# Optimization experiments

Measured on AMD Instinct MI355X. Metric: run time of the kernel, lower is better.

## Reference

```python
import jax, jax.numpy as jnp
import numpy as np

NGRAM = 16
SUB = 512  # bytes per sub-block


def byte2image(block, ngram=NGRAM):
    """block: (B, L) int -> (B, 1, ngram*8, L-ngram) float32 in [-1, 1]."""
    B, L = block.shape
    blk = block.astype(jnp.int32)
    # nxt[:, i] = blk[:, i+1], last column zero
    nxt = jnp.concatenate([blk[:, 1:], jnp.zeros((B, 1), jnp.int32)], axis=1)
    # 8 bit-shifted views of the byte stream
    shifts = jnp.stack(
        [((blk << s) & 255) + ((nxt >> (8 - s)) & 255) for s in range(8)],
        axis=1,
    )  # (B, 8, L)
    flat = shifts.reshape(B, -1)  # (B, 8*L)
    parts = [flat] + [jnp.roll(flat, -i, axis=1) for i in range(1, ngram)]
    stacked = jnp.concatenate(parts, axis=1).reshape(B, ngram * 8, L)
    result = stacked[:, :, :-ngram].astype(jnp.float32)
    result = (result / 255.0 - 0.5) / 0.5
    return result[:, None]  # (B, 1, ngram*8, L-ngram)


def byte2image_4k(block, ngram=NGRAM):
    """block: (B, 4096) -> (B, 8, ngram*8, 512-ngram)."""
    return jnp.concatenate(
        [byte2image(block[:, i * SUB:(i + 1) * SUB], ngram) for i in range(8)],
        axis=1,
    )


def setup_inputs() -> dict:
    key = jax.random.key(0)
    kx, kw = jax.random.split(key)
    x = jax.random.randint(kx, (256, 4096), 0, 256, dtype=jnp.int64)
    W = jax.random.normal(kw, (496, 64), dtype=jnp.float32) * 0.02
    return {"x": x, "W": W}


def reference(x, W):
    # ByteFormerWrapper.forward with block_size=4096: byte2image_4k then the
    # (opaque) model; model stood in by a linear head over the image width.
    img = byte2image_4k(x)                      # (B, 8, 128, 496)
    out = jnp.einsum('bchw,wo->bcho', img, W)   # (B, 8, 128, 64)
    return out
```

## Files before the change

kernel.cpp:

```cpp
#include <hip/hip_runtime.h>

typedef unsigned short u16;
typedef __attribute__((ext_vector_type(8))) short short8;
typedef __attribute__((ext_vector_type(4))) float floatx4;

#define WST 532
#define BST 136
#define KCHUNK 128

__device__ __forceinline__ u16 f2bf_rne(float f) {
  unsigned u = __float_as_uint(f);
  u += 0x7fffu + ((u >> 16) & 1u);
  return (u16)(u >> 16);
}

__global__ __launch_bounds__(256, 4) void byteformer_kernel(
    const int* __restrict__ x, const float* __restrict__ Wm,
    float* __restrict__ out) {
  __shared__ float wlds[8 * WST];
  __shared__ __align__(16) u16 Bt[64 * BST];
  __shared__ float part[256];
  __shared__ float csum[64];

  const int t = threadIdx.x;
  const int bid = blockIdx.x;
  const long xbase = (long)bid * 512;

  if (t < 8 * (WST - 512)) {
    int q = t / (WST - 512), mm = 512 + t % (WST - 512);
    wlds[q * WST + mm] = 0.0f;
  }
  #pragma unroll
  for (int half = 0; half < 2; ++half) {
    int m = t + 256 * half;
    int b0 = x[xbase + m] & 255;
    int b1 = (m == 511) ? 0 : (x[xbase + m + 1] & 255);
    #pragma unroll
    for (int q = 0; q < 8; ++q) {
      int wv = ((b0 << q) & 255) + (b1 >> (8 - q));
      wlds[q * WST + m] = (float)wv;
    }
  }

  const int wave = t >> 6;
  const int lane = t & 63;
  const int quad = lane >> 4;
  const int l16 = lane & 15;

  const int qa = l16 & 7;
  const int p0 = wave * 4 + (l16 >> 3);
  const int aBase = qa * WST + p0 + 8 * quad;

  floatx4 acc[2][4];
  #pragma unroll
  for (int mt = 0; mt < 2; ++mt)
    #pragma unroll
    for (int nt = 0; nt < 4; ++nt)
      acc[mt][nt] = floatx4{0.f, 0.f, 0.f, 0.f};

  float csum_local = 0.0f;
  const float scale = 2.0f / 255.0f;

  for (int kc = 0; kc < 4; ++kc) {
    __syncthreads();
    #pragma unroll
    for (int i = 0; i < 16; ++i) {
      int flat = t + 256 * i;
      int o = flat & 63;
      int kp = flat >> 6;
      int c0 = kc * KCHUNK + 2 * kp;
      float v0 = (c0 < 496) ? Wm[c0 * 64 + o] : 0.0f;
      float v1 = (c0 + 1 < 496) ? Wm[(c0 + 1) * 64 + o] : 0.0f;
      csum_local += v0 + v1;
      unsigned packed = (unsigned)f2bf_rne(v0 * scale) |
                        ((unsigned)f2bf_rne(v1 * scale) << 16);
      *((unsigned*)&Bt[o * BST + 2 * kp]) = packed;
    }
    __syncthreads();

    #pragma unroll
    for (int ks = 0; ks < 4; ++ks) {
      const int k0 = kc * KCHUNK + ks * 32;
      short8 afrag[2];
      #pragma unroll
      for (int mt = 0; mt < 2; ++mt) {
        const float* src = &wlds[aBase + mt * 2 + k0];
        short8 f;
        #pragma unroll
        for (int j = 0; j < 8; ++j)
          f[j] = (short)(__float_as_uint(src[j]) >> 16);
        afrag[mt] = f;
      }
      const int kloc = ks * 32 + 8 * quad;
      short8 bfrag[4];
      #pragma unroll
      for (int nt = 0; nt < 4; ++nt)
        bfrag[nt] = *((const short8*)&Bt[(nt * 16 + l16) * BST + kloc]);
      #pragma unroll
      for (int mt = 0; mt < 2; ++mt)
        #pragma unroll
        for (int nt = 0; nt < 4; ++nt)
          acc[mt][nt] = __builtin_amdgcn_mfma_f32_16x16x32_bf16(
              afrag[mt], bfrag[nt], acc[mt][nt], 0, 0, 0);
    }
  }

  part[t] = csum_local;
  __syncthreads();
  if (t < 64)
    csum[t] = part[t] + part[t + 64] + part[t + 128] + part[t + 192];
  __syncthreads();

  float* outb = out + (long)bid * (128 * 64);
  #pragma unroll
  for (int mt = 0; mt < 2; ++mt) {
    int r0 = wave * 32 + mt * 16 + quad * 4;
    #pragma unroll
    for (int nt = 0; nt < 4; ++nt) {
      int o = nt * 16 + l16;
      float cs = csum[o];
      #pragma unroll
      for (int i = 0; i < 4; ++i)
        outb[(long)(r0 + i) * 64 + o] = acc[mt][nt][i] - cs;
    }
  }
}

extern "C" void kernel_launch(void* const* d_in, const int* in_sizes, int n_in,
                              void* d_out, int out_size, void* d_ws, size_t ws_size,
                              hipStream_t stream) {
  const int* x = (const int*)d_in[0];
  const float* Wm = (const float*)d_in[1];
  float* out = (float*)d_out;
  byteformer_kernel<<<dim3(2048), dim3(256), 0, stream>>>(x, Wm, out);
}
```

Before: 117.1 us.

## Reformulate as Toeplitz-expanded weight GEMM with separate weight prep kernel

```diff
diff --git a/kernel.cpp b/kernel.cpp
--- a/kernel.cpp
+++ b/kernel.cpp
@@ -1,127 +1,140 @@
 #include <hip/hip_runtime.h>
 
 typedef unsigned short u16;
+typedef unsigned int u32;
 typedef __attribute__((ext_vector_type(8))) short short8;
 typedef __attribute__((ext_vector_type(4))) float floatx4;
 
-#define WST 532
-#define BST 136
-#define KCHUNK 128
+#define LSTRIDE 72
 
 __device__ __forceinline__ u16 f2bf_rne(float f) {
-  unsigned u = __float_as_uint(f);
+  u32 u = __float_as_uint(f);
   u += 0x7fffu + ((u >> 16) & 1u);
   return (u16)(u >> 16);
 }
+__device__ __forceinline__ short i2bf_exact(int v) {
+  return (short)(__float_as_uint((float)v) >> 16);
+}
 
-__global__ __launch_bounds__(256, 4) void byteformer_kernel(
-    const int* __restrict__ x, const float* __restrict__ Wm,
-    float* __restrict__ out) {
-  __shared__ float wlds[8 * WST];
-  __shared__ __align__(16) u16 Bt[64 * BST];
-  __shared__ float part[256];
-  __shared__ float csum[64];
+__global__ __launch_bounds__(256) void prep_kernel(const float* __restrict__ Wm,
+                                                   u16* __restrict__ Btg,
+                                                   float* __restrict__ csum_g) {
+  const int b = blockIdx.x;
+  const int t = threadIdx.x;
+  if (b < 256) {
+    int gid = b * 256 + t;
+    int o = gid & 63;
+    int rest = gid >> 6;
+    int m8 = rest & 63;
+    int p = rest >> 6;
+    const float scale = 2.0f / 255.0f;
+    short8 v;
+    #pragma unroll
+    for (int j = 0; j < 8; ++j) {
+      int c = m8 * 8 + j - p;
+      float f = (c >= 0 && c < 496) ? Wm[c * 64 + o] * scale : 0.0f;
+      v[j] = (short)f2bf_rne(f);
+    }
+    *(short8*)&Btg[((long)(p * 64 + o)) * 512 + m8 * 8] = v;
+  } else {
+    __shared__ float red[256];
+    int o = t & 63, seg = t >> 6;
+    float s = 0.0f;
+    for (int c = seg; c < 496; c += 4) s += Wm[c * 64 + o];
+    red[t] = s;
+    __syncthreads();
+    if (t < 64) csum_g[t] = red[t] + red[t + 64] + red[t + 128] + red[t + 192];
+  }
+}
+
+__global__ __launch_bounds__(256, 4) void gemm_kernel(
+    const int* __restrict__ x, const u16* __restrict__ Btg,
+    const float* __restrict__ csum_g, float* __restrict__ out) {
+  __shared__ __align__(16) u16 As[128 * LSTRIDE];
+  __shared__ __align__(16) u16 Bs[128 * LSTRIDE];
 
   const int t = threadIdx.x;
-  const int bid = blockIdx.x;
-  const long xbase = (long)bid * 512;
+  const int mtile = blockIdx.x;
+  const int n0 = blockIdx.y * 128;
 
-  if (t < 8 * (WST - 512)) {
-    int q = t / (WST - 512), mm = 512 + t % (WST - 512);
-    wlds[q * WST + mm] = 0.0f;
-  }
+  const int wave = t >> 6, lane = t & 63;
+  const int wm = wave >> 1, wn = wave & 1;
+  const int quad = lane >> 4, l16 = lane & 15;
+
+  const int sA_sub = t >> 4;
+  const int sA_kg  = (t >> 1) & 7;
+  const int sA_qh  = t & 1;
+  const long xrow = ((long)mtile * 16 + sA_sub) * 512;
+
+  floatx4 acc[4][4];
   #pragma unroll
-  for (int half = 0; half < 2; ++half) {
-    int m = t + 256 * half;
-    int b0 = x[xbase + m] & 255;
-    int b1 = (m == 511) ? 0 : (x[xbase + m + 1] & 255);
-    #pragma unroll
-    for (int q = 0; q < 8; ++q) {
-      int wv = ((b0 << q) & 255) + (b1 >> (8 - q));
-      wlds[q * WST + m] = (float)wv;
-    }
-  }
-
-  const int wave = t >> 6;
-  const int lane = t & 63;
-  const int quad = lane >> 4;
-  const int l16 = lane & 15;
-
-  const int qa = l16 & 7;
-  const int p0 = wave * 4 + (l16 >> 3);
-  const int aBase = qa * WST + p0 + 8 * quad;
-
-  floatx4 acc[2][4];
-  #pragma unroll
-  for (int mt = 0; mt < 2; ++mt)
+  for (int mt = 0; mt < 4; ++mt)
     #pragma unroll
     for (int nt = 0; nt < 4; ++nt)
       acc[mt][nt] = floatx4{0.f, 0.f, 0.f, 0.f};
 
-  float csum_local = 0.0f;
-  const float scale = 2.0f / 255.0f;
-
-  for (int kc = 0; kc < 4; ++kc) {
+  for (int kc = 0; kc < 8; ++kc) {
+    const int k0 = kc * 64;
+    __syncthreads();
+    {
+      const int base = k0 + sA_kg * 8;
+      int4 a0 = *(const int4*)&x[xrow + base];
+      int4 a1 = *(const int4*)&x[xrow + base + 4];
+      int c8 = (base + 8 < 512) ? x[xrow + base + 8] : 0;
+      int c[9] = {a0.x, a0.y, a0.z, a0.w, a1.x, a1.y, a1.z, a1.w, c8};
+      #pragma unroll
+      for (int qi = 0; qi < 4; ++qi) {
+        const int q = sA_qh * 4 + qi;
+        short8 w;
+        #pragma unroll
+        for (int j = 0; j < 8; ++j) {
+          int v = ((c[j] << q) & 255) + ((c[j + 1] & 255) >> (8 - q));
+          w[j] = i2bf_exact(v);
+        }
+        *(short8*)&As[(sA_sub * 8 + q) * LSTRIDE + sA_kg * 8] = w;
+      }
+    }
+    #pragma unroll
+    for (int pass = 0; pass < 4; ++pass) {
+      int flat = t + pass * 256;
+      int n = flat >> 3, kgl = flat & 7;
+      short8 bv = *(const short8*)&Btg[(long)(n0 + n) * 512 + k0 + kgl * 8];
+      *(short8*)&Bs[n * LSTRIDE + kgl * 8] = bv;
+    }
     __syncthreads();
     #pragma unroll
-    for (int i = 0; i < 16; ++i) {
-      int flat = t + 256 * i;
-      int o = flat & 63;
-      int kp = flat >> 6;
-      int c0 = kc * KCHUNK + 2 * kp;
-      float v0 = (c0 < 496) ? Wm[c0 * 64 + o] : 0.0f;
-      float v1 = (c0 + 1 < 496) ? Wm[(c0 + 1) * 64 + o] : 0.0f;
-      csum_local += v0 + v1;
-      unsigned packed = (unsigned)f2bf_rne(v0 * scale) |
-                        ((unsigned)f2bf_rne(v1 * scale) << 16);
-      *((unsigned*)&Bt[o * BST + 2 * kp]) = packed;
-    }
-    __syncthreads();
-
-    #pragma unroll
-    for (int ks = 0; ks < 4; ++ks) {
-      const int k0 = kc * KCHUNK + ks * 32;
-      short8 afrag[2];
+    for (int ks = 0; ks < 2; ++ks) {
+      const int koff = ks * 32 + quad * 8;
+      short8 af[4], bf[4];
       #pragma unroll
-      for (int mt = 0; mt < 2; ++mt) {
-        const float* src = &wlds[aBase + mt * 2 + k0];
-        short8 f;
-        #pragma unroll
-        for (int j = 0; j < 8; ++j)
-          f[j] = (short)(__float_as_uint(src[j]) >> 16);
-        afrag[mt] = f;
-      }
-      const int kloc = ks * 32 + 8 * quad;
-      short8 bfrag[4];
+      for (int mt = 0; mt < 4; ++mt)
+        af[mt] = *(const short8*)&As[(wm * 64 + mt * 16 + l16) * LSTRIDE + koff];
       #pragma unroll
       for (int nt = 0; nt < 4; ++nt)
-        bfrag[nt] = *((const short8*)&Bt[(nt * 16 + l16) * BST + kloc]);
+        bf[nt] = *(const short8*)&Bs[(wn * 64 + nt * 16 + l16) * LSTRIDE + koff];
       #pragma unroll
-      for (int mt = 0; mt < 2; ++mt)
+      for (int mt = 0; mt < 4; ++mt)
         #pragma unroll
         for (int nt = 0; nt < 4; ++nt)
           acc[mt][nt] = __builtin_amdgcn_mfma_f32_16x16x32_bf16(
-              afrag[mt], bfrag[nt], acc[mt][nt], 0, 0, 0);
+              af[mt], bf[nt], acc[mt][nt], 0, 0, 0);
     }
   }
 
-  part[t] = csum_local;
-  __syncthreads();
-  if (t < 64)
-    csum[t] = part[t] + part[t + 64] + part[t + 128] + part[t + 192];
-  __syncthreads();
-
-  float* outb = out + (long)bid * (128 * 64);
   #pragma unroll
-  for (int mt = 0; mt < 2; ++mt) {
-    int r0 = wave * 32 + mt * 16 + quad * 4;
+  for (int nt = 0; nt < 4; ++nt) {
+    int n = n0 + wn * 64 + nt * 16 + l16;
+    int p = n >> 6, o = n & 63;
+    float cs = csum_g[o];
     #pragma unroll
-    for (int nt = 0; nt < 4; ++nt) {
-      int o = nt * 16 + l16;
-      float cs = csum[o];
+    for (int mt = 0; mt < 4; ++mt) {
+      int mbase = mtile * 128 + wm * 64 + mt * 16 + quad * 4;
       #pragma unroll
-      for (int i = 0; i < 4; ++i)
-        outb[(long)(r0 + i) * 64 + o] = acc[mt][nt][i] - cs;
+      for (int i = 0; i < 4; ++i) {
+        int mr = mbase + i;
+        int bid = mr >> 3, q = mr & 7;
+        out[(long)bid * 8192 + (p * 8 + q) * 64 + o] = acc[mt][nt][i] - cs;
+      }
     }
   }
 }
@@ -132,5 +145,10 @@
   const int* x = (const int*)d_in[0];
   const float* Wm = (const float*)d_in[1];
   float* out = (float*)d_out;
-  byteformer_kernel<<<dim3(2048), dim3(256), 0, stream>>>(x, Wm, out);
+
+  u16* Btg = (u16*)d_ws;
+  float* csum_g = (float*)((char*)d_ws + (1u << 20));
+
+  prep_kernel<<<dim3(257), dim3(256), 0, stream>>>(Wm, Btg, csum_g);
+  gemm_kernel<<<dim3(128, 8), dim3(256), 0, stream>>>(x, Btg, csum_g, out);
 }
```

New measurement: 129.8 us. +10.8%, slower.
